# Optimization experiments

Measured on AMD Instinct MI355X. Metric: run time of the kernel, lower is better.

## Reference

```python
import jax, jax.numpy as jnp
import numpy as np

N, L, E, H = 4, 1024, 1024, 32
HD = E // H  # head_dim == heads by construction (32)


def setup_inputs() -> dict:
    key = jax.random.key(0)
    ks = jax.random.split(key, 8)
    values = jax.random.normal(ks[0], (N, L, E), dtype=jnp.float32)
    keys = jax.random.normal(ks[1], (N, L, E), dtype=jnp.float32)
    query = jax.random.normal(ks[2], (N, L, E), dtype=jnp.float32)
    mask = jnp.ones((N, 1, 1, L), dtype=jnp.int32)
    # per-head projection weights (torch Linear, no bias): y = x @ W.T
    s = 1.0 / np.sqrt(HD)
    Wv = jax.random.uniform(ks[3], (HD, HD), jnp.float32, -s, s)
    Wk = jax.random.uniform(ks[4], (HD, HD), jnp.float32, -s, s)
    Wq = jax.random.uniform(ks[5], (HD, HD), jnp.float32, -s, s)
    se = 1.0 / np.sqrt(E)
    Wo = jax.random.uniform(ks[6], (E, E), jnp.float32, -se, se)
    bo = jax.random.uniform(ks[7], (E,), jnp.float32, -se, se)
    return {"values": values, "keys": keys, "query": query, "mask": mask,
            "Wv": Wv, "Wk": Wk, "Wq": Wq, "Wo": Wo, "bo": bo}


def reference(values, keys, query, mask, Wv, Wk, Wq, Wo, bo):
    n = query.shape[0]
    # reshape (N, L, H, HD) then per-head linear projections (x @ W.T)
    v = values.reshape(n, -1, H, HD) @ Wv.T
    k = keys.reshape(n, -1, H, HD) @ Wk.T
    q = query.reshape(n, -1, H, HD) @ Wq.T
    # full score matrix [N, H, Q, K]
    energy = jnp.einsum('nqhd,nkhd->nhqk', q, k)
    energy = jnp.where(mask == 0, jnp.float32(-1e20), energy)
    attention = jax.nn.softmax(energy / jnp.sqrt(jnp.float32(E)), axis=3)
    out = jnp.einsum('nhql,nlhd->nqhd', attention, v)
    out = out.reshape(n, -1, H * HD)
    return out @ Wo.T + bo
```

## Files before the change

kernel.cpp:

```cpp
#include <hip/hip_runtime.h>
#include <hip/hip_bf16.h>

#define N_ 4
#define L_ 1024
#define E_ 1024
#define H_ 32
#define HD_ 32

typedef unsigned short ushort;
typedef __attribute__((ext_vector_type(8))) short short8;
typedef __attribute__((ext_vector_type(4))) short short4v;
typedef __attribute__((ext_vector_type(4))) float float4v;
typedef __attribute__((ext_vector_type(2))) unsigned int uint2v;

__device__ __forceinline__ ushort f2b(float f) {
    __hip_bfloat16 h = __float2bfloat16(f);
    return *reinterpret_cast<ushort*>(&h);
}

__device__ __forceinline__ unsigned packbf2(float a, float b) {
    unsigned ua = __float_as_uint(a);
    unsigned ub = __float_as_uint(b);
    ua += 0x7FFFu + ((ua >> 16) & 1u);
    ub += 0x7FFFu + ((ub >> 16) & 1u);
    return (ua >> 16) | (ub & 0xFFFF0000u);
}

__device__ __forceinline__ float fast_exp2(float x) {
#if __has_builtin(__builtin_amdgcn_exp2f)
    return __builtin_amdgcn_exp2f(x);
#else
    return __expf(x * 0.69314718056f);
#endif
}

__device__ __forceinline__ short8 cvt8(const float* __restrict__ p) {
    float4v a = *(const float4v*)p;
    float4v b = *(const float4v*)(p + 4);
    short8 r;
    r[0] = (short)f2b(a[0]); r[1] = (short)f2b(a[1]);
    r[2] = (short)f2b(a[2]); r[3] = (short)f2b(a[3]);
    r[4] = (short)f2b(b[0]); r[5] = (short)f2b(b[1]);
    r[6] = (short)f2b(b[2]); r[7] = (short)f2b(b[3]);
    return r;
}

__global__ __launch_bounds__(256) void convert_kernel(
    const float* __restrict__ Wv, const float* __restrict__ Wk,
    const float* __restrict__ Wq, const float* __restrict__ Wo,
    const int* __restrict__ mask,
    ushort* __restrict__ w3, ushort* __restrict__ wo_bf,
    float* __restrict__ bias_f)
{
    const int b = blockIdx.x, t = threadIdx.x;
    if (b == 0) {
        for (int i = t; i < 3 * HD_ * HD_; i += 256) {
            float v = (i < 1024) ? Wv[i] : (i < 2048 ? Wk[i - 1024] : Wq[i - 2048]);
            w3[i] = f2b(v);
        }
    } else if (b == 1) {
        for (int i = t; i < N_ * L_; i += 256)
            bias_f[i] = (mask[i] == 0) ? -1e30f : 0.0f;
    } else {
        int i = (b - 2) * 1024 + t * 4;
        float4v v = *(const float4v*)(Wo + i);
        short4v o;
        o[0] = (short)f2b(v[0]); o[1] = (short)f2b(v[1]);
        o[2] = (short)f2b(v[2]); o[3] = (short)f2b(v[3]);
        *(short4v*)(wo_bf + i) = o;
    }
}

__global__ __launch_bounds__(256) void proj_kernel(
    const float* __restrict__ v_in, const float* __restrict__ k_in,
    const float* __restrict__ q_in, const ushort* __restrict__ w3,
    ushort* __restrict__ vt_ws, ushort* __restrict__ k_ws,
    ushort* __restrict__ q_ws)
{
    const int n = blockIdx.z, h = blockIdx.y, l0 = blockIdx.x * 64;
    const int t = threadIdx.x, wave = t >> 6, lane = t & 63;
    const int m = lane & 15, g = lane >> 4;

    const size_t row = (size_t)(n * L_) + l0 + wave * 16 + m;
    const float* src[3] = {v_in, k_in, q_in};
    short8 A[3];
#pragma unroll
    for (int mat = 0; mat < 3; ++mat)
        A[mat] = cvt8(src[mat] + row * E_ + h * HD_ + g * 8);

    float4v acc[3][2];
#pragma unroll
    for (int mat = 0; mat < 3; ++mat)
#pragma unroll
        for (int dt = 0; dt < 2; ++dt) {
            short8 B = *(const short8*)(w3 + mat * 1024 + (dt * 16 + m) * HD_ + g * 8);
            float4v z = float4v{0.f, 0.f, 0.f, 0.f};
            acc[mat][dt] = __builtin_amdgcn_mfma_f32_16x16x32_bf16(A[mat], B, z, 0, 0, 0);
        }

    const size_t obase = (size_t)(n * H_ + h) * L_;
    const size_t vb = (size_t)(n * H_ + h) * HD_ * L_;
#pragma unroll
    for (int dt = 0; dt < 2; ++dt)
#pragma unroll
        for (int r = 0; r < 4; ++r) {
            int tok = l0 + wave * 16 + g * 4 + r;
            int d = dt * 16 + m;
            k_ws[(obase + tok) * HD_ + d] = f2b(acc[1][dt][r]);
            q_ws[(obase + tok) * HD_ + d] = f2b(acc[2][dt][r]);
            vt_ws[vb + (size_t)d * L_ + tok] = f2b(acc[0][dt][r]);
        }
}

__global__ __launch_bounds__(256, 4) void attn_kernel(
    const ushort* __restrict__ q_ws, const ushort* __restrict__ k_ws,
    const ushort* __restrict__ vt_ws, const float* __restrict__ bias_f,
    ushort* __restrict__ x_ws)
{
    const int B = blockIdx.x;
    const int head = ((B >> 6) << 3) + (B & 7);
    const int qt = (B >> 3) & 7;
    const int n = head >> 5, h = head & 31, q0 = qt * 128;

    const int t = threadIdx.x, wave = t >> 6, lane = t & 63;
    const int m = lane & 15, g = lane >> 4;

    __shared__ ushort sP[4][2][16][72];

    const size_t base = (size_t)(n * H_ + h) * L_;
    const ushort* vb_p = vt_ws + (size_t)(n * H_ + h) * HD_ * L_;

    short8 qfa = *(const short8*)(q_ws + (base + q0 + wave * 16 + m) * HD_ + g * 8);
    short8 qfb = *(const short8*)(q_ws + (base + q0 + 64 + wave * 16 + m) * HD_ + g * 8);

    float4v Oa[2], Ob[2];
    Oa[0] = float4v{0.f,0.f,0.f,0.f}; Oa[1] = float4v{0.f,0.f,0.f,0.f};
    Ob[0] = float4v{0.f,0.f,0.f,0.f}; Ob[1] = float4v{0.f,0.f,0.f,0.f};
    float rsa[4] = {0.f,0.f,0.f,0.f}, rsb[4] = {0.f,0.f,0.f,0.f};
    const float k1 = 0.03125f * 1.44269504f;

    ushort* pa = &sP[wave][0][m][0];
    ushort* pb = &sP[wave][1][m][0];

    const ushort* kp  = k_ws + base * HD_ + (size_t)m * HD_ + g * 8;
    const ushort* vp  = vb_p + (size_t)m * L_ + g * 8;
    const float*  bp  = bias_f + n * L_ + g * 4;

    short8 kf[4];
#pragma unroll
    for (int nb = 0; nb < 4; ++nb)
        kf[nb] = *(const short8*)(kp + (size_t)nb * 16 * HD_);
    kp += (size_t)64 * HD_;

    for (int c = 0; c < 16; ++c) {
        float4v Sa[4], Sb[4];
#pragma unroll
        for (int nb = 0; nb < 4; ++nb) {
            float4v z = float4v{0.f,0.f,0.f,0.f};
            Sa[nb] = __builtin_amdgcn_mfma_f32_16x16x32_bf16(kf[nb], qfa, z, 0, 0, 0);
        }
#pragma unroll
        for (int nb = 0; nb < 4; ++nb) {
            float4v z = float4v{0.f,0.f,0.f,0.f};
            Sb[nb] = __builtin_amdgcn_mfma_f32_16x16x32_bf16(kf[nb], qfb, z, 0, 0, 0);
        }
#pragma unroll
        for (int nb = 0; nb < 4; ++nb)
            kf[nb] = *(const short8*)(kp + (size_t)nb * 16 * HD_);
        kp += (size_t)64 * HD_;
        short8 vf[2][2];
#pragma unroll
        for (int kb = 0; kb < 2; ++kb)
#pragma unroll
            for (int db = 0; db < 2; ++db)
                vf[kb][db] = *(const short8*)(vp + (size_t)db * 16 * L_ + kb * 32);
        vp += 64;

#pragma unroll
        for (int nb = 0; nb < 4; ++nb) {
            float4v b4 = *(const float4v*)(bp + nb * 16);
            float a0 = fast_exp2(fmaf(Sa[nb][0], k1, b4[0]));
            float a1 = fast_exp2(fmaf(Sa[nb][1], k1, b4[1]));
            float a2 = fast_exp2(fmaf(Sa[nb][2], k1, b4[2]));
            float a3 = fast_exp2(fmaf(Sa[nb][3], k1, b4[3]));
            rsa[0] += a0; rsa[1] += a1; rsa[2] += a2; rsa[3] += a3;
            uint2v pka; pka[0] = packbf2(a0, a1); pka[1] = packbf2(a2, a3);
            *(uint2v*)(pa + nb * 16 + g * 4) = pka;
            float e0 = fast_exp2(fmaf(Sb[nb][0], k1, b4[0]));
            float e1 = fast_exp2(fmaf(Sb[nb][1], k1, b4[1]));
            float e2 = fast_exp2(fmaf(Sb[nb][2], k1, b4[2]));
            float e3 = fast_exp2(fmaf(Sb[nb][3], k1, b4[3]));
            rsb[0] += e0; rsb[1] += e1; rsb[2] += e2; rsb[3] += e3;
            uint2v pkb; pkb[0] = packbf2(e0, e1); pkb[1] = packbf2(e2, e3);
            *(uint2v*)(pb + nb * 16 + g * 4) = pkb;
        }
        bp += 64;

#pragma unroll
        for (int kb = 0; kb < 2; ++kb) {
            short8 af = *(const short8*)(pa + kb * 32 + g * 8);
            Oa[0] = __builtin_amdgcn_mfma_f32_16x16x32_bf16(af, vf[kb][0], Oa[0], 0, 0, 0);
            Oa[1] = __builtin_amdgcn_mfma_f32_16x16x32_bf16(af, vf[kb][1], Oa[1], 0, 0, 0);
        }
#pragma unroll
        for (int kb = 0; kb < 2; ++kb) {
            short8 bf = *(const short8*)(pb + kb * 32 + g * 8);
            Ob[0] = __builtin_amdgcn_mfma_f32_16x16x32_bf16(bf, vf[kb][0], Ob[0], 0, 0, 0);
            Ob[1] = __builtin_amdgcn_mfma_f32_16x16x32_bf16(bf, vf[kb][1], Ob[1], 0, 0, 0);
        }
    }

    float ra = (rsa[0] + rsa[1]) + (rsa[2] + rsa[3]);
    float rb = (rsb[0] + rsb[1]) + (rsb[2] + rsb[3]);
    ra += __shfl_xor(ra, 16, 64); ra += __shfl_xor(ra, 32, 64);
    rb += __shfl_xor(rb, 16, 64); rb += __shfl_xor(rb, 32, 64);
#pragma unroll
    for (int r = 0; r < 4; ++r) {
        float inva = 1.f / __shfl(ra, g * 4 + r, 64);
        float invb = 1.f / __shfl(rb, g * 4 + r, 64);
        size_t rowa = (size_t)n * L_ + q0 + wave * 16 + g * 4 + r;
        size_t rowb = rowa + 64;
#pragma unroll
        for (int db = 0; db < 2; ++db) {
            x_ws[rowa * E_ + h * HD_ + db * 16 + m] = f2b(Oa[db][r] * inva);
            x_ws[rowb * E_ + h * HD_ + db * 16 + m] = f2b(Ob[db][r] * invb);
        }
    }
}

__global__ __launch_bounds__(256) void out_gemm_kernel(
    const ushort* __restrict__ X, const ushort* __restrict__ wo_bf,
    const float* __restrict__ bo, float* __restrict__ C)
{
    const int B = blockIdx.x;
    const int it = ((B >> 7) << 3) + (B & 7);
    const int jt = (B >> 3) & 15;
    const int i0 = it * 64, j0 = jt * 64;

    const int t = threadIdx.x, wave = t >> 6, lane = t & 63;
    const int m = lane & 15, g = lane >> 4;

    __shared__ ushort sA[64][72];
    __shared__ ushort sB[64][72];

    float4v acc[4];
#pragma unroll
    for (int nb = 0; nb < 4; ++nb) acc[nb] = float4v{0.f,0.f,0.f,0.f};

    const int r0 = t >> 2;
    const int c0 = (t & 3) * 16;

    for (int k0 = 0; k0 < E_; k0 += 64) {
        __syncthreads();
        *(short8*)&sA[r0][c0]     = *(const short8*)(X + (size_t)(i0 + r0) * E_ + k0 + c0);
        *(short8*)&sA[r0][c0 + 8] = *(const short8*)(X + (size_t)(i0 + r0) * E_ + k0 + c0 + 8);
        *(short8*)&sB[r0][c0]     = *(const short8*)(wo_bf + (size_t)(j0 + r0) * E_ + k0 + c0);
        *(short8*)&sB[r0][c0 + 8] = *(const short8*)(wo_bf + (size_t)(j0 + r0) * E_ + k0 + c0 + 8);
        __syncthreads();
#pragma unroll
        for (int kb = 0; kb < 2; ++kb) {
            short8 afr = *(const short8*)&sA[wave * 16 + m][kb * 32 + g * 8];
#pragma unroll
            for (int nb = 0; nb < 4; ++nb) {
                short8 bfr = *(const short8*)&sB[nb * 16 + m][kb * 32 + g * 8];
                acc[nb] = __builtin_amdgcn_mfma_f32_16x16x32_bf16(afr, bfr, acc[nb], 0, 0, 0);
            }
        }
    }

#pragma unroll
    for (int nb = 0; nb < 4; ++nb) {
        int col = j0 + nb * 16 + m;
        float bias = bo[col];
#pragma unroll
        for (int r = 0; r < 4; ++r) {
            int rowi = i0 + wave * 16 + g * 4 + r;
            C[(size_t)rowi * E_ + col] = acc[nb][r] + bias;
        }
    }
}

extern "C" void kernel_launch(void* const* d_in, const int* in_sizes, int n_in,
                              void* d_out, int out_size, void* d_ws, size_t ws_size,
                              hipStream_t stream) {
    const float* values = (const float*)d_in[0];
    const float* keys   = (const float*)d_in[1];
    const float* query  = (const float*)d_in[2];
    const int*   mask   = (const int*)d_in[3];
    const float* Wv     = (const float*)d_in[4];
    const float* Wk     = (const float*)d_in[5];
    const float* Wq     = (const float*)d_in[6];
    const float* Wo     = (const float*)d_in[7];
    const float* bo     = (const float*)d_in[8];
    float* out = (float*)d_out;

    const size_t M4 = (size_t)N_ * H_ * L_ * HD_;
    ushort* q_ws   = (ushort*)d_ws;
    ushort* k_ws   = q_ws + M4;
    ushort* vt_ws  = k_ws + M4;
    ushort* x_ws   = vt_ws + M4;
    ushort* wo_bf  = x_ws + M4;
    ushort* w3     = wo_bf + (size_t)E_ * E_;
    float*  bias_f = (float*)(w3 + 3 * HD_ * HD_);

    convert_kernel<<<dim3(2 + (E_ * E_) / 1024), 256, 0, stream>>>(
        Wv, Wk, Wq, Wo, mask, w3, wo_bf, bias_f);

    proj_kernel<<<dim3(L_ / 64, H_, N_), 256, 0, stream>>>(
        values, keys, query, w3, vt_ws, k_ws, q_ws);

    attn_kernel<<<dim3(1024), 256, 0, stream>>>(
        q_ws, k_ws, vt_ws, bias_f, x_ws);

    out_gemm_kernel<<<dim3(1024), 256, 0, stream>>>(
        x_ws, wo_bf, bo, out);
}
```

Before: 192.8 us.

## Fuse weight conversion into consumers and software-pipeline attention and output GEMM

Removes the separate convert kernel. Weight and mask conversion now happens inside the projection kernel, and Wo is converted to bf16 on the fly while staging into shared memory in the output GEMM. The attention loop is restructured with a double-buffered P tile so the PV MFMAs of the previous chunk overlap the QK and exp of the current one. The output GEMM also register-prefetches its next tile, and the V projection is computed transposed so stores are contiguous. The trade-off is redundant conversion of Wo in every output GEMM block (fp32 reads double that traffic) and more shared memory in attention.

```diff
diff --git a/kernel.cpp b/kernel.cpp
--- a/kernel.cpp
+++ b/kernel.cpp
@@ -9,14 +9,8 @@
 
 typedef unsigned short ushort;
 typedef __attribute__((ext_vector_type(8))) short short8;
-typedef __attribute__((ext_vector_type(4))) short short4v;
 typedef __attribute__((ext_vector_type(4))) float float4v;
 typedef __attribute__((ext_vector_type(2))) unsigned int uint2v;
-
-__device__ __forceinline__ ushort f2b(float f) {
-    __hip_bfloat16 h = __float2bfloat16(f);
-    return *reinterpret_cast<ushort*>(&h);
-}
 
 __device__ __forceinline__ unsigned packbf2(float a, float b) {
     unsigned ua = __float_as_uint(a);
@@ -26,6 +20,12 @@
     return (ua >> 16) | (ub & 0xFFFF0000u);
 }
 
+__device__ __forceinline__ ushort f2b(float f) {
+    unsigned u = __float_as_uint(f);
+    u += 0x7FFFu + ((u >> 16) & 1u);
+    return (ushort)(u >> 16);
+}
+
 __device__ __forceinline__ float fast_exp2(float x) {
 #if __has_builtin(__builtin_amdgcn_exp2f)
     return __builtin_amdgcn_exp2f(x);
@@ -37,79 +37,67 @@
 __device__ __forceinline__ short8 cvt8(const float* __restrict__ p) {
     float4v a = *(const float4v*)p;
     float4v b = *(const float4v*)(p + 4);
-    short8 r;
-    r[0] = (short)f2b(a[0]); r[1] = (short)f2b(a[1]);
-    r[2] = (short)f2b(a[2]); r[3] = (short)f2b(a[3]);
-    r[4] = (short)f2b(b[0]); r[5] = (short)f2b(b[1]);
-    r[6] = (short)f2b(b[2]); r[7] = (short)f2b(b[3]);
-    return r;
-}
-
-__global__ __launch_bounds__(256) void convert_kernel(
-    const float* __restrict__ Wv, const float* __restrict__ Wk,
-    const float* __restrict__ Wq, const float* __restrict__ Wo,
-    const int* __restrict__ mask,
-    ushort* __restrict__ w3, ushort* __restrict__ wo_bf,
-    float* __restrict__ bias_f)
-{
-    const int b = blockIdx.x, t = threadIdx.x;
-    if (b == 0) {
-        for (int i = t; i < 3 * HD_ * HD_; i += 256) {
-            float v = (i < 1024) ? Wv[i] : (i < 2048 ? Wk[i - 1024] : Wq[i - 2048]);
-            w3[i] = f2b(v);
-        }
-    } else if (b == 1) {
-        for (int i = t; i < N_ * L_; i += 256)
-            bias_f[i] = (mask[i] == 0) ? -1e30f : 0.0f;
-    } else {
-        int i = (b - 2) * 1024 + t * 4;
-        float4v v = *(const float4v*)(Wo + i);
-        short4v o;
-        o[0] = (short)f2b(v[0]); o[1] = (short)f2b(v[1]);
-        o[2] = (short)f2b(v[2]); o[3] = (short)f2b(v[3]);
-        *(short4v*)(wo_bf + i) = o;
-    }
+    union { unsigned u[4]; short8 s; } r;
+    r.u[0] = packbf2(a[0], a[1]); r.u[1] = packbf2(a[2], a[3]);
+    r.u[2] = packbf2(b[0], b[1]); r.u[3] = packbf2(b[2], b[3]);
+    return r.s;
 }
 
 __global__ __launch_bounds__(256) void proj_kernel(
     const float* __restrict__ v_in, const float* __restrict__ k_in,
-    const float* __restrict__ q_in, const ushort* __restrict__ w3,
+    const float* __restrict__ q_in,
+    const float* __restrict__ Wv, const float* __restrict__ Wk,
+    const float* __restrict__ Wq, const int* __restrict__ mask,
     ushort* __restrict__ vt_ws, ushort* __restrict__ k_ws,
-    ushort* __restrict__ q_ws)
+    ushort* __restrict__ q_ws, float* __restrict__ bias_f)
 {
     const int n = blockIdx.z, h = blockIdx.y, l0 = blockIdx.x * 64;
     const int t = threadIdx.x, wave = t >> 6, lane = t & 63;
     const int m = lane & 15, g = lane >> 4;
 
+    if (h == 0 && t < 64)
+        bias_f[n * L_ + l0 + t] = (mask[n * L_ + l0 + t] == 0) ? -1e30f : 0.0f;
+
     const size_t row = (size_t)(n * L_) + l0 + wave * 16 + m;
     const float* src[3] = {v_in, k_in, q_in};
-    short8 A[3];
-#pragma unroll
-    for (int mat = 0; mat < 3; ++mat)
-        A[mat] = cvt8(src[mat] + row * E_ + h * HD_ + g * 8);
-
-    float4v acc[3][2];
-#pragma unroll
-    for (int mat = 0; mat < 3; ++mat)
-#pragma unroll
-        for (int dt = 0; dt < 2; ++dt) {
-            short8 B = *(const short8*)(w3 + mat * 1024 + (dt * 16 + m) * HD_ + g * 8);
-            float4v z = float4v{0.f, 0.f, 0.f, 0.f};
-            acc[mat][dt] = __builtin_amdgcn_mfma_f32_16x16x32_bf16(A[mat], B, z, 0, 0, 0);
-        }
+    const float* wsrc[3] = {Wv, Wk, Wq};
+
+    short8 Xf[3], Wf[3][2];
+#pragma unroll
+    for (int mat = 0; mat < 3; ++mat) {
+        Xf[mat] = cvt8(src[mat] + row * E_ + h * HD_ + g * 8);
+#pragma unroll
+        for (int dt = 0; dt < 2; ++dt)
+            Wf[mat][dt] = cvt8(wsrc[mat] + (dt * 16 + m) * HD_ + g * 8);
+    }
 
     const size_t obase = (size_t)(n * H_ + h) * L_;
     const size_t vb = (size_t)(n * H_ + h) * HD_ * L_;
-#pragma unroll
-    for (int dt = 0; dt < 2; ++dt)
+
+#pragma unroll
+    for (int mat = 1; mat < 3; ++mat) {
+        ushort* outp = (mat == 1) ? k_ws : q_ws;
+#pragma unroll
+        for (int dt = 0; dt < 2; ++dt) {
+            float4v z = float4v{0.f, 0.f, 0.f, 0.f};
+            float4v acc = __builtin_amdgcn_mfma_f32_16x16x32_bf16(Xf[mat], Wf[mat][dt], z, 0, 0, 0);
+#pragma unroll
+            for (int r = 0; r < 4; ++r) {
+                int tok = l0 + wave * 16 + g * 4 + r;
+                outp[(obase + tok) * HD_ + dt * 16 + m] = f2b(acc[r]);
+            }
+        }
+    }
+#pragma unroll
+    for (int dt = 0; dt < 2; ++dt) {
+        float4v z = float4v{0.f, 0.f, 0.f, 0.f};
+        float4v acc = __builtin_amdgcn_mfma_f32_16x16x32_bf16(Wf[0][dt], Xf[0], z, 0, 0, 0);
 #pragma unroll
         for (int r = 0; r < 4; ++r) {
-            int tok = l0 + wave * 16 + g * 4 + r;
-            int d = dt * 16 + m;
-            k_ws[(obase + tok) * HD_ + d] = f2b(acc[1][dt][r]);
-            q_ws[(obase + tok) * HD_ + d] = f2b(acc[2][dt][r]);
-            vt_ws[vb + (size_t)d * L_ + tok] = f2b(acc[0][dt][r]);
-        }
+            int d = dt * 16 + g * 4 + r;
+            vt_ws[vb + (size_t)d * L_ + l0 + wave * 16 + m] = f2b(acc[r]);
+        }
+    }
 }
 
 __global__ __launch_bounds__(256, 4) void attn_kernel(
@@ -125,7 +113,7 @@
     const int t = threadIdx.x, wave = t >> 6, lane = t & 63;
     const int m = lane & 15, g = lane >> 4;
 
-    __shared__ ushort sP[4][2][16][72];
+    __shared__ ushort sP[4][2][2][16][72];
 
     const size_t base = (size_t)(n * H_ + h) * L_;
     const ushort* vb_p = vt_ws + (size_t)(n * H_ + h) * HD_ * L_;
@@ -139,12 +127,14 @@
     float rsa[4] = {0.f,0.f,0.f,0.f}, rsb[4] = {0.f,0.f,0.f,0.f};
     const float k1 = 0.03125f * 1.44269504f;
 
-    ushort* pa = &sP[wave][0][m][0];
-    ushort* pb = &sP[wave][1][m][0];
-
-    const ushort* kp  = k_ws + base * HD_ + (size_t)m * HD_ + g * 8;
-    const ushort* vp  = vb_p + (size_t)m * L_ + g * 8;
-    const float*  bp  = bias_f + n * L_ + g * 4;
+    ushort* const pa0 = &sP[wave][0][0][m][0];
+    ushort* const pa1 = &sP[wave][1][0][m][0];
+    ushort* const pb0 = &sP[wave][0][1][m][0];
+    ushort* const pb1 = &sP[wave][1][1][m][0];
+
+    const ushort* kp = k_ws + base * HD_ + (size_t)m * HD_ + g * 8;
+    const ushort* vp = vb_p + (size_t)m * L_ + g * 8;
+    const float*  bp = bias_f + n * L_ + g * 4;
 
     short8 kf[4];
 #pragma unroll
@@ -152,30 +142,75 @@
         kf[nb] = *(const short8*)(kp + (size_t)nb * 16 * HD_);
     kp += (size_t)64 * HD_;
 
-    for (int c = 0; c < 16; ++c) {
-        float4v Sa[4], Sb[4];
+    float4v Sa[4], Sb[4];
+#pragma unroll
+    for (int nb = 0; nb < 4; ++nb) {
+        float4v z = float4v{0.f,0.f,0.f,0.f};
+        Sa[nb] = __builtin_amdgcn_mfma_f32_16x16x32_bf16(kf[nb], qfa, z, 0, 0, 0);
+        Sb[nb] = __builtin_amdgcn_mfma_f32_16x16x32_bf16(kf[nb], qfb, z, 0, 0, 0);
+    }
+#pragma unroll
+    for (int nb = 0; nb < 4; ++nb)
+        kf[nb] = *(const short8*)(kp + (size_t)nb * 16 * HD_);
+    kp += (size_t)64 * HD_;
+#pragma unroll
+    for (int nb = 0; nb < 4; ++nb) {
+        float4v b4 = *(const float4v*)(bp + nb * 16);
+        float a0 = fast_exp2(fmaf(Sa[nb][0], k1, b4[0]));
+        float a1 = fast_exp2(fmaf(Sa[nb][1], k1, b4[1]));
+        float a2 = fast_exp2(fmaf(Sa[nb][2], k1, b4[2]));
+        float a3 = fast_exp2(fmaf(Sa[nb][3], k1, b4[3]));
+        rsa[0] += a0; rsa[1] += a1; rsa[2] += a2; rsa[3] += a3;
+        uint2v pk; pk[0] = packbf2(a0, a1); pk[1] = packbf2(a2, a3);
+        *(uint2v*)(pa0 + nb * 16 + g * 4) = pk;
+        float e0 = fast_exp2(fmaf(Sb[nb][0], k1, b4[0]));
+        float e1 = fast_exp2(fmaf(Sb[nb][1], k1, b4[1]));
+        float e2 = fast_exp2(fmaf(Sb[nb][2], k1, b4[2]));
+        float e3 = fast_exp2(fmaf(Sb[nb][3], k1, b4[3]));
+        rsb[0] += e0; rsb[1] += e1; rsb[2] += e2; rsb[3] += e3;
+        uint2v qk; qk[0] = packbf2(e0, e1); qk[1] = packbf2(e2, e3);
+        *(uint2v*)(pb0 + nb * 16 + g * 4) = qk;
+    }
+    bp += 64;
+
+    for (int c = 1; c < 16; ++c) {
+        short8 vf[2][2];
+#pragma unroll
+        for (int kb = 0; kb < 2; ++kb)
+#pragma unroll
+            for (int db = 0; db < 2; ++db)
+                vf[kb][db] = *(const short8*)(vp + (size_t)db * 16 * L_ + kb * 32);
+        vp += 64;
+
 #pragma unroll
         for (int nb = 0; nb < 4; ++nb) {
             float4v z = float4v{0.f,0.f,0.f,0.f};
             Sa[nb] = __builtin_amdgcn_mfma_f32_16x16x32_bf16(kf[nb], qfa, z, 0, 0, 0);
-        }
-#pragma unroll
-        for (int nb = 0; nb < 4; ++nb) {
-            float4v z = float4v{0.f,0.f,0.f,0.f};
             Sb[nb] = __builtin_amdgcn_mfma_f32_16x16x32_bf16(kf[nb], qfb, z, 0, 0, 0);
         }
+
+        const ushort* ra = (c & 1) ? pa0 : pa1;
+        const ushort* rb = (c & 1) ? pb0 : pb1;
+#pragma unroll
+        for (int kb = 0; kb < 2; ++kb) {
+            short8 af = *(const short8*)(ra + kb * 32 + g * 8);
+            Oa[0] = __builtin_amdgcn_mfma_f32_16x16x32_bf16(af, vf[kb][0], Oa[0], 0, 0, 0);
+            Oa[1] = __builtin_amdgcn_mfma_f32_16x16x32_bf16(af, vf[kb][1], Oa[1], 0, 0, 0);
+        }
+#pragma unroll
+        for (int kb = 0; kb < 2; ++kb) {
+            short8 bf = *(const short8*)(rb + kb * 32 + g * 8);
+            Ob[0] = __builtin_amdgcn_mfma_f32_16x16x32_bf16(bf, vf[kb][0], Ob[0], 0, 0, 0);
+            Ob[1] = __builtin_amdgcn_mfma_f32_16x16x32_bf16(bf, vf[kb][1], Ob[1], 0, 0, 0);
+        }
+
 #pragma unroll
         for (int nb = 0; nb < 4; ++nb)
             kf[nb] = *(const short8*)(kp + (size_t)nb * 16 * HD_);
         kp += (size_t)64 * HD_;
-        short8 vf[2][2];
-#pragma unroll
-        for (int kb = 0; kb < 2; ++kb)
-#pragma unroll
-            for (int db = 0; db < 2; ++db)
-                vf[kb][db] = *(const short8*)(vp + (size_t)db * 16 * L_ + kb * 32);
-        vp += 64;
-
+
+        ushort* wa = (c & 1) ? pa1 : pa0;
+        ushort* wb = (c & 1) ? pb1 : pb0;
 #pragma unroll
         for (int nb = 0; nb < 4; ++nb) {
             float4v b4 = *(const float4v*)(bp + nb * 16);
@@ -184,27 +219,35 @@
             float a2 = fast_exp2(fmaf(Sa[nb][2], k1, b4[2]));
             float a3 = fast_exp2(fmaf(Sa[nb][3], k1, b4[3]));
             rsa[0] += a0; rsa[1] += a1; rsa[2] += a2; rsa[3] += a3;
-            uint2v pka; pka[0] = packbf2(a0, a1); pka[1] = packbf2(a2, a3);
-            *(uint2v*)(pa + nb * 16 + g * 4) = pka;
+            uint2v pk; pk[0] = packbf2(a0, a1); pk[1] = packbf2(a2, a3);
+            *(uint2v*)(wa + nb * 16 + g * 4) = pk;
             float e0 = fast_exp2(fmaf(Sb[nb][0], k1, b4[0]));
             float e1 = fast_exp2(fmaf(Sb[nb][1], k1, b4[1]));
             float e2 = fast_exp2(fmaf(Sb[nb][2], k1, b4[2]));
             float e3 = fast_exp2(fmaf(Sb[nb][3], k1, b4[3]));
             rsb[0] += e0; rsb[1] += e1; rsb[2] += e2; rsb[3] += e3;
-            uint2v pkb; pkb[0] = packbf2(e0, e1); pkb[1] = packbf2(e2, e3);
-            *(uint2v*)(pb + nb * 16 + g * 4) = pkb;
+            uint2v qk; qk[0] = packbf2(e0, e1); qk[1] = packbf2(e2, e3);
+            *(uint2v*)(wb + nb * 16 + g * 4) = qk;
         }
         bp += 64;
-
-#pragma unroll
-        for (int kb = 0; kb < 2; ++kb) {
-            short8 af = *(const short8*)(pa + kb * 32 + g * 8);
+    }
+
+    {
+        short8 vf[2][2];
+#pragma unroll
+        for (int kb = 0; kb < 2; ++kb)
+#pragma unroll
+            for (int db = 0; db < 2; ++db)
+                vf[kb][db] = *(const short8*)(vp + (size_t)db * 16 * L_ + kb * 32);
+#pragma unroll
+        for (int kb = 0; kb < 2; ++kb) {
+            short8 af = *(const short8*)(pa1 + kb * 32 + g * 8);
             Oa[0] = __builtin_amdgcn_mfma_f32_16x16x32_bf16(af, vf[kb][0], Oa[0], 0, 0, 0);
             Oa[1] = __builtin_amdgcn_mfma_f32_16x16x32_bf16(af, vf[kb][1], Oa[1], 0, 0, 0);
         }
 #pragma unroll
         for (int kb = 0; kb < 2; ++kb) {
-            short8 bf = *(const short8*)(pb + kb * 32 + g * 8);
+            short8 bf = *(const short8*)(pb1 + kb * 32 + g * 8);
             Ob[0] = __builtin_amdgcn_mfma_f32_16x16x32_bf16(bf, vf[kb][0], Ob[0], 0, 0, 0);
             Ob[1] = __builtin_amdgcn_mfma_f32_16x16x32_bf16(bf, vf[kb][1], Ob[1], 0, 0, 0);
         }
@@ -229,7 +272,7 @@
 }
 
 __global__ __launch_bounds__(256) void out_gemm_kernel(
-    const ushort* __restrict__ X, const ushort* __restrict__ wo_bf,
+    const ushort* __restrict__ X, const float* __restrict__ Wo,
     const float* __restrict__ bo, float* __restrict__ C)
 {
     const int B = blockIdx.x;
@@ -250,13 +293,36 @@
     const int r0 = t >> 2;
     const int c0 = (t & 3) * 16;
 
+    const ushort* xp = X + (size_t)(i0 + r0) * E_ + c0;
+    const float*  wp = Wo + (size_t)(j0 + r0) * E_ + c0;
+
+    short8 xr0 = *(const short8*)xp;
+    short8 xr1 = *(const short8*)(xp + 8);
+    float4v wr0 = *(const float4v*)wp;
+    float4v wr1 = *(const float4v*)(wp + 4);
+    float4v wr2 = *(const float4v*)(wp + 8);
+    float4v wr3 = *(const float4v*)(wp + 12);
+
     for (int k0 = 0; k0 < E_; k0 += 64) {
         __syncthreads();
-        *(short8*)&sA[r0][c0]     = *(const short8*)(X + (size_t)(i0 + r0) * E_ + k0 + c0);
-        *(short8*)&sA[r0][c0 + 8] = *(const short8*)(X + (size_t)(i0 + r0) * E_ + k0 + c0 + 8);
-        *(short8*)&sB[r0][c0]     = *(const short8*)(wo_bf + (size_t)(j0 + r0) * E_ + k0 + c0);
-        *(short8*)&sB[r0][c0 + 8] = *(const short8*)(wo_bf + (size_t)(j0 + r0) * E_ + k0 + c0 + 8);
+        *(short8*)&sA[r0][c0]     = xr0;
+        *(short8*)&sA[r0][c0 + 8] = xr1;
+        union { unsigned u[4]; short8 s; } b0, b1;
+        b0.u[0] = packbf2(wr0[0], wr0[1]); b0.u[1] = packbf2(wr0[2], wr0[3]);
+        b0.u[2] = packbf2(wr1[0], wr1[1]); b0.u[3] = packbf2(wr1[2], wr1[3]);
+        b1.u[0] = packbf2(wr2[0], wr2[1]); b1.u[1] = packbf2(wr2[2], wr2[3]);
+        b1.u[2] = packbf2(wr3[0], wr3[1]); b1.u[3] = packbf2(wr3[2], wr3[3]);
+        *(short8*)&sB[r0][c0]     = b0.s;
+        *(short8*)&sB[r0][c0 + 8] = b1.s;
         __syncthreads();
+        if (k0 + 64 < E_) {
+            xr0 = *(const short8*)(xp + k0 + 64);
+            xr1 = *(const short8*)(xp + k0 + 72);
+            wr0 = *(const float4v*)(wp + k0 + 64);
+            wr1 = *(const float4v*)(wp + k0 + 68);
+            wr2 = *(const float4v*)(wp + k0 + 72);
+            wr3 = *(const float4v*)(wp + k0 + 76);
+        }
 #pragma unroll
         for (int kb = 0; kb < 2; ++kb) {
             short8 afr = *(const short8*)&sA[wave * 16 + m][kb * 32 + g * 8];
@@ -299,19 +365,14 @@
     ushort* k_ws   = q_ws + M4;
     ushort* vt_ws  = k_ws + M4;
     ushort* x_ws   = vt_ws + M4;
-    ushort* wo_bf  = x_ws + M4;
-    ushort* w3     = wo_bf + (size_t)E_ * E_;
-    float*  bias_f = (float*)(w3 + 3 * HD_ * HD_);
-
-    convert_kernel<<<dim3(2 + (E_ * E_) / 1024), 256, 0, stream>>>(
-        Wv, Wk, Wq, Wo, mask, w3, wo_bf, bias_f);
+    float*  bias_f = (float*)(x_ws + M4);
 
     proj_kernel<<<dim3(L_ / 64, H_, N_), 256, 0, stream>>>(
-        values, keys, query, w3, vt_ws, k_ws, q_ws);
+        values, keys, query, Wv, Wk, Wq, mask, vt_ws, k_ws, q_ws, bias_f);
 
     attn_kernel<<<dim3(1024), 256, 0, stream>>>(
         q_ws, k_ws, vt_ws, bias_f, x_ws);
 
     out_gemm_kernel<<<dim3(1024), 256, 0, stream>>>(
-        x_ws, wo_bf, bo, out);
-}
+        x_ws, Wo, bo, out);
+}
```

New measurement: 198.8 us. 1.03x slower.
